# Optimization experiments

Measured on AMD Instinct MI355X. Metric: run time of the kernel, lower is better.

## Reference

```python
import jax, jax.numpy as jnp
import numpy as np

N, L, D, W = 64, 514, 768, 256   # batch, padded token len (incl CLS/SEP), bert dim, max words
H1, H2 = 500, 300                # linear1 out, out_size
LN_EPS = 1e-5


def setup_inputs() -> dict:
    key = jax.random.key(0)
    ks = jax.random.split(key, 6)
    texts = jax.random.normal(ks[0], (N, L, D), dtype=jnp.float32)
    # contiguous ragged spans: lengths in {1,2}, cumulative ends <= 512 = L-2 always
    lens = jax.random.randint(ks[1], (N, W), 1, 3)
    word_ends = jnp.cumsum(lens, axis=1).astype(jnp.int32)
    word_starts = (word_ends - lens).astype(jnp.int32)
    word_length = jax.random.randint(ks[2], (N,), W // 2, W + 1).astype(jnp.int32)
    W1 = jax.random.normal(ks[3], (D, H1), dtype=jnp.float32) * np.float32(1.0 / np.sqrt(D))
    b1 = jnp.zeros((H1,), jnp.float32)
    W2 = jax.random.normal(ks[4], (H1, H2), dtype=jnp.float32) * np.float32(1.0 / np.sqrt(H1))
    b2 = jnp.zeros((H2,), jnp.float32)
    gamma = jnp.ones((H2,), jnp.float32)
    beta = jnp.zeros((H2,), jnp.float32)
    return dict(texts=texts, word_starts=word_starts, word_ends=word_ends,
                word_length=word_length, W1=W1, b1=b1, W2=W2, b2=b2,
                gamma=gamma, beta=beta)


def reference(texts, word_starts, word_ends, word_length, W1, b1, W2, b2, gamma, beta):
    # texts: (N, L, D) BERT output; drop [CLS]/[SEP]
    tok = texts[:, 1:-1, :]  # (N, L-2, D)
    # offset-based segment mean: prefix sums over token axis
    csum = jnp.concatenate([jnp.zeros_like(tok[:, :1]), jnp.cumsum(tok, axis=1)], axis=1)  # (N, L-1, D)
    e = word_ends[:, :, None].astype(jnp.int32)
    s = word_starts[:, :, None].astype(jnp.int32)
    seg_sum = jnp.take_along_axis(csum, e, axis=1) - jnp.take_along_axis(csum, s, axis=1)  # (N, W, D)
    cnt = (word_ends - word_starts).astype(texts.dtype)[:, :, None]
    pooled = seg_sum / jnp.maximum(cnt, 1.0)
    # pad_sequence semantics: words beyond word_length[i] are zero
    mask = (jnp.arange(W)[None, :] < word_length[:, None])[:, :, None]
    pooled = jnp.where(mask, pooled, jnp.zeros((), texts.dtype))
    # MLP + LayerNorm: norm(relu(linear2(relu(linear1(x)))))
    h = jax.nn.relu(pooled @ W1 + b1)
    h = jax.nn.relu(h @ W2 + b2)
    mu = jnp.mean(h, axis=-1, keepdims=True)
    var = jnp.mean(jnp.square(h - mu), axis=-1, keepdims=True)
    return (h - mu) * jax.lax.rsqrt(var + LN_EPS) * gamma + beta  # (N, W, 300)
```

## Files before the change

### kernel.cpp

```cpp
#include <hip/hip_runtime.h>
#include <hip/hip_bf16.h>


#define N_  64
#define L_  514
#define D_  768
#define W_  256
#define H1_ 500
#define H1P 512
#define H2_ 300
#define H2P 320
#define LN_EPS 1e-5f
#define M_  (N_ * W_)

typedef __bf16 bf16x8 __attribute__((ext_vector_type(8)));
typedef float  f32x4  __attribute__((ext_vector_type(4)));

__device__ __forceinline__ void load_lds16(const void* g, void* l) {
    __builtin_amdgcn_global_load_lds(
        (const __attribute__((address_space(1))) void*)g,
        (__attribute__((address_space(3))) void*)l, 16, 0, 0);
}

#define CONV1_ELEMS (H1P * D_)
#define CONV2_ELEMS (H2P * H1P)
#define CONV1_B ((CONV1_ELEMS + 191) / 192)
#define CONV2_B ((CONV2_ELEMS + 191) / 192)

__global__ __launch_bounds__(192) void prep_kernel(
    const float* __restrict__ texts, const int* __restrict__ wstart,
    const int* __restrict__ wend, const int* __restrict__ wlen,
    const float* __restrict__ W1, const float* __restrict__ W2,
    __hip_bfloat16* __restrict__ pooled, __hip_bfloat16* __restrict__ W1T,
    __hip_bfloat16* __restrict__ W2T)
{
    int b = blockIdx.x;
    if (b < M_) {
        int n = b >> 8;
        int w = b & (W_ - 1);
        int s = wstart[b], e = wend[b];
        bool live = (w < wlen[n]);
        int d = threadIdx.x * 4;
        float4 acc = make_float4(0.f, 0.f, 0.f, 0.f);
        if (live) {
            const float* base = texts + ((size_t)n * L_ + 1) * D_ + d;
            for (int i = s; i < e; ++i) {
                float4 v = *reinterpret_cast<const float4*>(base + (size_t)i * D_);
                acc.x += v.x; acc.y += v.y; acc.z += v.z; acc.w += v.w;
            }
            float inv = 1.0f / (float)max(e - s, 1);
            acc.x *= inv; acc.y *= inv; acc.z *= inv; acc.w *= inv;
        }
        union { __hip_bfloat16 h[4]; uint2 u; } o;
        o.h[0] = __float2bfloat16(acc.x); o.h[1] = __float2bfloat16(acc.y);
        o.h[2] = __float2bfloat16(acc.z); o.h[3] = __float2bfloat16(acc.w);
        *reinterpret_cast<uint2*>(pooled + (size_t)b * D_ + d) = o.u;
    } else if (b < M_ + CONV1_B) {
        int t = (b - M_) * 192 + threadIdx.x;
        if (t < CONV1_ELEMS) {
            int n = t / D_, k = t - n * D_;
            float v = (n < H1_) ? W1[(size_t)k * H1_ + n] : 0.f;
            W1T[t] = __float2bfloat16(v);
        }
    } else {
        int t = (b - M_ - CONV1_B) * 192 + threadIdx.x;
        if (t < CONV2_ELEMS) {
            int n = t >> 9, k = t & (H1P - 1);
            float v = (n < H2_ && k < H1_) ? W2[(size_t)k * H2_ + n] : 0.f;
            W2T[t] = __float2bfloat16(v);
        }
    }
}

__global__ __launch_bounds__(512, 1) void gemm1_kernel(
    const ushort* __restrict__ A, const ushort* __restrict__ B,
    const float* __restrict__ b1, ushort* __restrict__ h1)
{
    constexpr int BUFB = 49152;
    __shared__ __align__(16) char bufs[3 * BUFB];
    const int tid  = threadIdx.x;
    const int wave = tid >> 6, lane = tid & 63;
    const int wm = wave >> 1, wn = wave & 1;
    const int t256 = (blockIdx.x & 7) * 32 + (blockIdx.x >> 3);
    const int bm = (t256 >> 2) * 256, bn = (t256 & 3) * 128;
    const int lrow8 = lane >> 3, lslot8 = lane & 7;
    const int g = lane >> 4, fr = lane & 15;

    f32x4 acc[4][4] = {};

    auto stage = [&](int buf, int kt) {
        char* base = bufs + buf * BUFB;
        #pragma unroll
        for (int c0 = 0; c0 < 6; ++c0) {
            int c = wave + c0 * 8;
            int row; const ushort* src;
            if (c < 32) { row = c * 8 + lrow8;        src = A + (size_t)(bm + row) * D_; }
            else        { row = (c - 32) * 8 + lrow8; src = B + (size_t)(bn + row) * D_; }
            int sslot = lslot8 ^ (row & 7);
            load_lds16(src + kt + sslot * 8, base + c * 1024);
        }
    };

    auto compute = [&](int t) {
        const char* base = bufs + (t % 3) * BUFB;
        #pragma unroll
        for (int h = 0; h < 2; ++h) {
            bf16x8 af[4], bf[4];
            #pragma unroll
            for (int mi = 0; mi < 4; ++mi) {
                int r = wm * 64 + mi * 16 + fr;
                af[mi] = *(const bf16x8*)(base + r * 128 + ((((h << 2) + g) ^ (r & 7)) << 4));
            }
            #pragma unroll
            for (int ni = 0; ni < 4; ++ni) {
                int r = wn * 64 + ni * 16 + fr;
                bf[ni] = *(const bf16x8*)(base + 32768 + r * 128 + ((((h << 2) + g) ^ (r & 7)) << 4));
            }
            __builtin_amdgcn_s_setprio(1);
            #pragma unroll
            for (int mi = 0; mi < 4; ++mi)
                #pragma unroll
                for (int ni = 0; ni < 4; ++ni)
                    acc[mi][ni] = __builtin_amdgcn_mfma_f32_16x16x32_bf16(
                        af[mi], bf[ni], acc[mi][ni], 0, 0, 0);
            __builtin_amdgcn_s_setprio(0);
        }
    };

    stage(0, 0); stage(1, 64);
    for (int t = 0; t < 11; ++t) {
        asm volatile("s_waitcnt vmcnt(6)" ::: "memory");
        __builtin_amdgcn_s_barrier();
        if (t + 2 < 12) stage((t + 2) % 3, (t + 2) * 64);
        compute(t);
    }
    asm volatile("s_waitcnt vmcnt(0)" ::: "memory");
    __builtin_amdgcn_s_barrier();
    compute(11);

    #pragma unroll
    for (int mi = 0; mi < 4; ++mi)
        #pragma unroll
        for (int ni = 0; ni < 4; ++ni) {
            int col = bn + wn * 64 + ni * 16 + fr;
            float bv = (col < H1_) ? b1[col] : 0.f;
            #pragma unroll
            for (int j = 0; j < 4; ++j) {
                int row = bm + wm * 64 + mi * 16 + g * 4 + j;
                float v = acc[mi][ni][j] + bv;
                ((__hip_bfloat16*)h1)[(size_t)row * H1P + col] =
                    __float2bfloat16(v > 0.f ? v : 0.f);
            }
        }
}

__global__ __launch_bounds__(512, 1) void gemm2_ln_kernel(
    const ushort* __restrict__ A, const ushort* __restrict__ B,
    const float* __restrict__ b2, const float* __restrict__ gamma,
    const float* __restrict__ beta, float* __restrict__ out)
{
    constexpr int BUFB = 24576;
    __shared__ __align__(16) char bufs[4 * BUFB];
    __shared__ float red[2][32][4][2];
    const int tid  = threadIdx.x;
    const int wave = tid >> 6, lane = tid & 63;
    const int wm = wave >> 2, wn = wave & 3;
    const int bm = blockIdx.x * 64;
    const int lrow = lane >> 2, lslot = lane & 3;
    const int g = lane >> 4, fr = lane & 15;

    f32x4 acc[2][5] = {};

    auto stage = [&](int buf, int kt) {
        char* base = bufs + buf * BUFB;
        #pragma unroll
        for (int c0 = 0; c0 < 3; ++c0) {
            int c = wave + c0 * 8;
            int row; const ushort* src;
            if (c < 4) { row = c * 16 + lrow; src = A + (size_t)(bm + row) * H1P; }
            else       { row = (c - 4) * 16 + lrow; src = B + (size_t)row * H1P; }
            int sslot = lslot ^ ((row >> 1) & 3);
            load_lds16(src + kt + sslot * 8, base + c * 1024);
        }
    };

    auto compute = [&](int t) {
        const char* base = bufs + (t & 3) * BUFB;
        bf16x8 af[2], bf[5];
        #pragma unroll
        for (int mi = 0; mi < 2; ++mi) {
            int r = wm * 32 + mi * 16 + fr;
            af[mi] = *(const bf16x8*)(base + r * 64 + ((g ^ ((r >> 1) & 3)) << 4));
        }
        #pragma unroll
        for (int ni = 0; ni < 5; ++ni) {
            int r = wn * 80 + ni * 16 + fr;
            bf[ni] = *(const bf16x8*)(base + 4096 + r * 64 + ((g ^ ((r >> 1) & 3)) << 4));
        }
        __builtin_amdgcn_s_setprio(1);
        #pragma unroll
        for (int mi = 0; mi < 2; ++mi)
            #pragma unroll
            for (int ni = 0; ni < 5; ++ni)
                acc[mi][ni] = __builtin_amdgcn_mfma_f32_16x16x32_bf16(
                    af[mi], bf[ni], acc[mi][ni], 0, 0, 0);
        __builtin_amdgcn_s_setprio(0);
    };

    stage(0, 0); stage(1, 32); stage(2, 64);
    for (int t = 0; t < 14; ++t) {
        asm volatile("s_waitcnt vmcnt(6)" ::: "memory");
        __builtin_amdgcn_s_barrier();
        if (t + 3 < 16) stage((t + 3) & 3, (t + 3) * 32);
        compute(t);
    }
    asm volatile("s_waitcnt vmcnt(3)" ::: "memory");
    __builtin_amdgcn_s_barrier();
    compute(14);
    asm volatile("s_waitcnt vmcnt(0)" ::: "memory");
    __builtin_amdgcn_s_barrier();
    compute(15);

    float vals[2][5][4];
    float rsum[2][4] = {}, rsq[2][4] = {};
    #pragma unroll
    for (int ni = 0; ni < 5; ++ni) {
        int col = wn * 80 + ni * 16 + fr;
        float bv = (col < H2_) ? b2[col] : 0.f;
        #pragma unroll
        for (int mi = 0; mi < 2; ++mi)
            #pragma unroll
            for (int j = 0; j < 4; ++j) {
                float v = acc[mi][ni][j] + bv;
                v = v > 0.f ? v : 0.f;
                vals[mi][ni][j] = v;
                rsum[mi][j] += v;
                rsq[mi][j]  += v * v;
            }
    }
    #pragma unroll
    for (int off = 1; off < 16; off <<= 1)
        #pragma unroll
        for (int mi = 0; mi < 2; ++mi)
            #pragma unroll
            for (int j = 0; j < 4; ++j) {
                rsum[mi][j] += __shfl_xor(rsum[mi][j], off);
                rsq[mi][j]  += __shfl_xor(rsq[mi][j], off);
            }
    if (fr == 0) {
        #pragma unroll
        for (int mi = 0; mi < 2; ++mi)
            #pragma unroll
            for (int j = 0; j < 4; ++j) {
                int r32 = mi * 16 + g * 4 + j;
                red[wm][r32][wn][0] = rsum[mi][j];
                red[wm][r32][wn][1] = rsq[mi][j];
            }
    }
    __syncthreads();
    #pragma unroll
    for (int mi = 0; mi < 2; ++mi) {
        #pragma unroll
        for (int j = 0; j < 4; ++j) {
            int r32 = mi * 16 + g * 4 + j;
            float S  = red[wm][r32][0][0] + red[wm][r32][1][0]
                     + red[wm][r32][2][0] + red[wm][r32][3][0];
            float SQ = red[wm][r32][0][1] + red[wm][r32][1][1]
                     + red[wm][r32][2][1] + red[wm][r32][3][1];
            float mu   = S * (1.0f / H2_);
            float var  = SQ * (1.0f / H2_) - mu * mu;
            float rstd = rsqrtf(var + LN_EPS);
            int row = bm + wm * 32 + r32;
            #pragma unroll
            for (int ni = 0; ni < 5; ++ni) {
                int col = wn * 80 + ni * 16 + fr;
                if (col < H2_)
                    out[(size_t)row * H2_ + col] =
                        (vals[mi][ni][j] - mu) * rstd * gamma[col] + beta[col];
            }
        }
    }
}

extern "C" void kernel_launch(void* const* d_in, const int* in_sizes, int n_in,
                              void* d_out, int out_size, void* d_ws, size_t ws_size,
                              hipStream_t stream)
{
    const float* texts  = (const float*)d_in[0];
    const int*   wstart = (const int*)  d_in[1];
    const int*   wend   = (const int*)  d_in[2];
    const int*   wlen   = (const int*)  d_in[3];
    const float* W1     = (const float*)d_in[4];
    const float* b1     = (const float*)d_in[5];
    const float* W2     = (const float*)d_in[6];
    const float* b2     = (const float*)d_in[7];
    const float* gamma  = (const float*)d_in[8];
    const float* beta   = (const float*)d_in[9];
    float* out = (float*)d_out;

    ushort* pooled = (ushort*)d_ws;
    ushort* h1     = pooled + (size_t)M_ * D_;
    ushort* W1T    = h1 + (size_t)M_ * H1P;
    ushort* W2T    = W1T + (size_t)H1P * D_;

    prep_kernel<<<M_ + CONV1_B + CONV2_B, 192, 0, stream>>>(
        texts, wstart, wend, wlen, W1, W2,
        (__hip_bfloat16*)pooled, (__hip_bfloat16*)W1T, (__hip_bfloat16*)W2T);

    gemm1_kernel<<<256, 512, 0, stream>>>(pooled, W1T, b1, h1);

    gemm2_ln_kernel<<<M_ / 64, 512, 0, stream>>>(h1, W2T, b2, gamma, beta, out);
}
```

Measured before the change: 55.89 us.

## Pool four words per block and transpose weights through LDS tiles

The prep kernel now assigns one wave per word and four words per 256-thread block, so each lane accumulates three float4 slices. This cuts the block count and the per-block overhead of pooling. The W1/W2 transpose-and-convert now goes through a padded 32x33 shared-memory tile, so both the global reads and the global writes are coalesced instead of strided. The cost is an extra __syncthreads and LDS use in the transpose blocks.

Result: no change. 55.16 us (median of 2 runs) (-1.3%).

```diff
diff --git a/kernel.cpp b/kernel.cpp
--- a/kernel.cpp
+++ b/kernel.cpp
@@ -22,52 +22,82 @@
         (__attribute__((address_space(3))) void*)l, 16, 0, 0);
 }
 
-#define CONV1_ELEMS (H1P * D_)
-#define CONV2_ELEMS (H2P * H1P)
-#define CONV1_B ((CONV1_ELEMS + 191) / 192)
-#define CONV2_B ((CONV2_ELEMS + 191) / 192)
-
-__global__ __launch_bounds__(192) void prep_kernel(
+__device__ __forceinline__ uint2 pack4(f32x4 v) {
+    union { __hip_bfloat16 h[4]; uint2 u; } o;
+    o.h[0] = __float2bfloat16(v[0]); o.h[1] = __float2bfloat16(v[1]);
+    o.h[2] = __float2bfloat16(v[2]); o.h[3] = __float2bfloat16(v[3]);
+    return o.u;
+}
+
+#define POOL_B (M_ / 4)
+#define CW1_B  (24 * 16)
+#define CW2_B  (16 * 10)
+
+__global__ __launch_bounds__(256) void prep_kernel(
     const float* __restrict__ texts, const int* __restrict__ wstart,
     const int* __restrict__ wend, const int* __restrict__ wlen,
     const float* __restrict__ W1, const float* __restrict__ W2,
     __hip_bfloat16* __restrict__ pooled, __hip_bfloat16* __restrict__ W1T,
     __hip_bfloat16* __restrict__ W2T)
 {
+    __shared__ float tile[32][33];
     int b = blockIdx.x;
-    if (b < M_) {
-        int n = b >> 8;
-        int w = b & (W_ - 1);
-        int s = wstart[b], e = wend[b];
-        bool live = (w < wlen[n]);
-        int d = threadIdx.x * 4;
-        float4 acc = make_float4(0.f, 0.f, 0.f, 0.f);
+    if (b < POOL_B) {
+        const int wave = threadIdx.x >> 6, lane = threadIdx.x & 63;
+        const int idx = b * 4 + wave;
+        const int n = idx >> 8, w = idx & (W_ - 1);
+        const int s = wstart[idx], e = wend[idx];
+        const bool live = (w < wlen[n]);
+        const float inv = live ? 1.0f / (float)max(e - s, 1) : 0.f;
+        f32x4 a0 = {}, a1 = {}, a2 = {};
         if (live) {
-            const float* base = texts + ((size_t)n * L_ + 1) * D_ + d;
-            for (int i = s; i < e; ++i) {
-                float4 v = *reinterpret_cast<const float4*>(base + (size_t)i * D_);
-                acc.x += v.x; acc.y += v.y; acc.z += v.z; acc.w += v.w;
-            }
-            float inv = 1.0f / (float)max(e - s, 1);
-            acc.x *= inv; acc.y *= inv; acc.z *= inv; acc.w *= inv;
-        }
-        union { __hip_bfloat16 h[4]; uint2 u; } o;
-        o.h[0] = __float2bfloat16(acc.x); o.h[1] = __float2bfloat16(acc.y);
-        o.h[2] = __float2bfloat16(acc.z); o.h[3] = __float2bfloat16(acc.w);
-        *reinterpret_cast<uint2*>(pooled + (size_t)b * D_ + d) = o.u;
-    } else if (b < M_ + CONV1_B) {
-        int t = (b - M_) * 192 + threadIdx.x;
-        if (t < CONV1_ELEMS) {
-            int n = t / D_, k = t - n * D_;
-            float v = (n < H1_) ? W1[(size_t)k * H1_ + n] : 0.f;
-            W1T[t] = __float2bfloat16(v);
+            const float* base = texts + ((size_t)n * L_ + 1 + s) * D_ + lane * 4;
+            for (int r = 0; r < e - s; ++r) {
+                const float* p = base + (size_t)r * D_;
+                a0 += *(const f32x4*)(p);
+                a1 += *(const f32x4*)(p + 256);
+                a2 += *(const f32x4*)(p + 512);
+            }
+            a0 *= inv; a1 *= inv; a2 *= inv;
+        }
+        __hip_bfloat16* dst = pooled + (size_t)idx * D_ + lane * 4;
+        *(uint2*)(dst)       = pack4(a0);
+        *(uint2*)(dst + 256) = pack4(a1);
+        *(uint2*)(dst + 512) = pack4(a2);
+    } else if (b < POOL_B + CW1_B) {
+        int t = b - POOL_B;
+        int kt = t % 24, nt = t / 24;
+        int r = threadIdx.x >> 5, c = threadIdx.x & 31;
+        #pragma unroll
+        for (int i = 0; i < 4; ++i) {
+            int kk = kt * 32 + r + i * 8;
+            int nn = nt * 32 + c;
+            tile[r + i * 8][c] = (nn < H1_) ? W1[(size_t)kk * H1_ + nn] : 0.f;
+        }
+        __syncthreads();
+        #pragma unroll
+        for (int i = 0; i < 4; ++i) {
+            int nn = nt * 32 + r + i * 8;
+            int kk = kt * 32 + c;
+            W1T[(size_t)nn * D_ + kk] = __float2bfloat16(tile[c][r + i * 8]);
         }
     } else {
-        int t = (b - M_ - CONV1_B) * 192 + threadIdx.x;
-        if (t < CONV2_ELEMS) {
-            int n = t >> 9, k = t & (H1P - 1);
-            float v = (n < H2_ && k < H1_) ? W2[(size_t)k * H2_ + n] : 0.f;
-            W2T[t] = __float2bfloat16(v);
+        int t = b - POOL_B - CW1_B;
+        int kt = t % 16, nt = t / 16;
+        int r = threadIdx.x >> 5, c = threadIdx.x & 31;
+        #pragma unroll
+        for (int i = 0; i < 4; ++i) {
+            int kk = kt * 32 + r + i * 8;
+            int nn = nt * 32 + c;
+            tile[r + i * 8][c] =
+                (nn < H2_ && kk < H1_) ? W2[(size_t)kk * H2_ + nn] : 0.f;
+        }
+        __syncthreads();
+        #pragma unroll
+        for (int i = 0; i < 4; ++i) {
+            int nn = nt * 32 + r + i * 8;
+            int kk = kt * 32 + c;
+            W2T[(size_t)nn * H1P + kk] = __float2bfloat16(tile[c][r + i * 8]);
         }
     }
 }
@@ -303,7 +333,7 @@
     ushort* W1T    = h1 + (size_t)M_ * H1P;
     ushort* W2T    = W1T + (size_t)H1P * D_;
 
-    prep_kernel<<<M_ + CONV1_B + CONV2_B, 192, 0, stream>>>(
+    prep_kernel<<<POOL_B + CW1_B + CW2_B, 256, 0, stream>>>(
         texts, wstart, wend, wlen, W1, W2,
         (__hip_bfloat16*)pooled, (__hip_bfloat16*)W1T, (__hip_bfloat16*)W2T);
 
```
